# Optimization experiments

Measured on AMD Instinct MI355X. Metric: run time of the kernel, lower is better.

## Reference

```python
import jax, jax.numpy as jnp
import numpy as np

ALPHA = 0.2  # LeakyReLU negative slope


def setup_inputs() -> dict:
    key = jax.random.key(0)
    k0, k1, k2, k3 = jax.random.split(key, 4)
    N, H, W, T, V = 16, 32, 32, 16, 64
    h = jax.random.normal(k0, (N, H, W, T, V), jnp.float32)
    conv_w = jax.random.normal(k1, (3, 3, T, T), jnp.float32) * 0.05  # HWIO
    conv_b = jnp.zeros((T,), jnp.float32)
    a = jax.random.normal(k2, (2 * H * W, 1), jnp.float32) * 0.03  # ~xavier scale
    B = jax.random.uniform(k3, (V, V), jnp.float32)
    return {"h": h, "conv_w": conv_w, "conv_b": conv_b, "a": a, "B": B}


def reference(h, conv_w, conv_b, a, B):
    N, H, W, T, V = h.shape
    hv = jnp.transpose(h, (0, 4, 1, 2, 3))  # (N,V,H,W,T)

    # ConvMapping: 3x3 SAME conv over spatial dims with T as channels
    x = hv.reshape(N * V, H, W, T)
    y = jax.lax.conv_general_dilated(
        x, conv_w, (1, 1), 'SAME',
        dimension_numbers=('NHWC', 'HWIO', 'NHWC')) + conv_b
    Wh = y.reshape(N, V, H, W, T)

    # Attention logits. Original builds concat([Wh_i, Wh_j], dim=W) with trailing
    # layout (H, 2W, T) then row-major views it as (T, 2*H*W). We reproduce that
    # exact reinterpretation, but exploit additivity over i/j so the O(V^2)
    # pair tensor is never materialized.
    HW2 = 2 * H * W
    zeros = jnp.zeros_like(Wh)
    Cl = jnp.concatenate([Wh, zeros], axis=3).reshape(N, V, T, HW2)
    Cr = jnp.concatenate([zeros, Wh], axis=3).reshape(N, V, T, HW2)
    av = a[:, 0]
    Ei = jnp.einsum('bvtk,k->bvt', Cl, av)
    Ej = jnp.einsum('bvtk,k->bvt', Cr, av)
    e = jax.nn.leaky_relu(Ei[:, :, None, :] + Ej[:, None, :, :], ALPHA)  # (N,V,V,T)
    att = jax.nn.softmax(e, axis=-1)  # softmax over time dim, as in original

    # Symmetric-normalized adjacency: D^-1/2 (B + I, min-max scaled) D^-1/2
    adj = B + jnp.eye(V, dtype=B.dtype)
    adj = (adj - adj.min()) / (adj.max() - adj.min())
    d12 = 1.0 / jnp.sqrt(jnp.sum(adj, axis=1))
    adj_norm = adj * d12[:, None] * d12[None, :]

    # Aggregation: h_prime[b,p,t,i] = sum_j Wh[b,j,p,t] * att[b,i,j,t]
    # (replaces the original V^2 python loop + diag_embed matmuls)
    Whf = Wh.reshape(N, V, H * W, T)
    hp = jnp.einsum('bjpt,bijt->bpti', Whf, att)  # (N,HW,T,V)
    out = jnp.einsum('bpti,iv->bptv', hp, adj_norm)
    return jax.nn.elu(out.reshape(N, H, W, T, V))
```

## Files before the change

### kernel.cpp

```cpp
#include <hip/hip_runtime.h>
#include <hip/hip_bf16.h>
#include <math.h>

#define ALPHA_ 0.2f
#define N_ 16
#define H_ 32
#define W_ 32
#define T_ 16
#define V_ 64
#define P_ (H_*W_)

typedef __bf16 bf16x8 __attribute__((ext_vector_type(8)));
typedef float  f32x4  __attribute__((ext_vector_type(4)));

static __device__ inline bf16x8 zero8() {
    bf16x8 z;
    #pragma unroll
    for (int i = 0; i < 8; ++i) z[i] = (__bf16)0.f;
    return z;
}

static __device__ inline unsigned short bf16bits(float f) {
    __hip_bfloat16 b = __float2bfloat16(f);
    return *reinterpret_cast<unsigned short*>(&b);
}

static __device__ inline __bf16 tobf(float f) {
    unsigned short u = bf16bits(f);
    return *reinterpret_cast<__bf16*>(&u);
}

__global__ __launch_bounds__(256) void conv_k(const float* __restrict__ X,
                                              const float* __restrict__ CW,
                                              const float* __restrict__ CB,
                                              const float* __restrict__ av,
                                              __hip_bfloat16* __restrict__ Whb,
                                              float* __restrict__ Eihi,
                                              float* __restrict__ Eihj) {
    __shared__ __align__(16) __hip_bfloat16 sx[3*32*2*16*8];
    __shared__ float sEi[4][16], sEj[4][16];

    int orig = blockIdx.x;
    int bi   = (orig & 7) * 256 + (orig >> 3);
    int b    = bi >> 7;
    int rem  = bi & 127;
    int h    = rem >> 2;
    int vg   = rem & 3, vb = vg * 16;

    int tid = threadIdx.x, lane = tid & 63, wc = tid >> 6;
    int lm = lane & 15, kg = lane >> 4;

    bf16x8 Bf01[3], Bf2[3];
    #pragma unroll
    for (int dw = 0; dw < 3; ++dw) {
        #pragma unroll
        for (int i = 0; i < 8; ++i) {
            int ti = (kg & 1)*8 + i;
            int dh = kg >> 1;
            Bf01[dw][i] = tobf(CW[((dh*3+dw)*16+ti)*16 + lm]);
            Bf2 [dw][i] = (kg < 2) ? tobf(CW[((6+dw)*16+ti)*16 + lm]) : (__bf16)0.f;
        }
    }
    float cb = CB[lm];
    f32x4 acc[8];
    #pragma unroll
    for (int wi = 0; wi < 8; ++wi) acc[wi] = (f32x4){cb, cb, cb, cb};

    unsigned* sxw = (unsigned*)sx;
    int v4i = tid & 3, tiP = (tid >> 2) & 7, sub = tid >> 5;
    const float* Xbase = X + (size_t)b*(H_*W_*T_*V_) + (size_t)(2*tiP)*V_ + vb + v4i*4;
    #pragma unroll
    for (int it = 0; it < 12; ++it) {
        int rest = it*8 + sub;
        int w = rest & 31, r = rest >> 5;
        int hy = h - 1 + r;
        f32x4 xa = {0.f,0.f,0.f,0.f}, xb = {0.f,0.f,0.f,0.f};
        if ((unsigned)hy < (unsigned)H_) {
            const float* p = Xbase + ((size_t)hy*W_ + w)*(T_*V_);
            xa = *(const f32x4*)(p);
            xb = *(const f32x4*)(p + V_);
        }
        int widx = ((r*32 + w)*2 + (tiP>>2))*64 + v4i*16 + (tiP & 3);
        #pragma unroll
        for (int k2 = 0; k2 < 4; ++k2) {
            unsigned pk = (unsigned)bf16bits(xa[k2]) | ((unsigned)bf16bits(xb[k2]) << 16);
            sxw[widx + k2*4] = pk;
        }
    }
    __syncthreads();

    const char* sxb = (const char*)sx;
    int off01 = (kg>>1)*16384 + (kg&1)*256 + lm*16;
    int off2  = 2*16384       + (kg&1)*256 + lm*16;

    #pragma unroll
    for (int u = 0; u < 10; ++u) {
        int wxu = wc*8 + u - 1;
        bf16x8 f01 = zero8(), f2 = zero8();
        if ((unsigned)wxu < (unsigned)W_) {
            f01 = *(const bf16x8*)(sxb + off01 + wxu*512);
            f2  = *(const bf16x8*)(sxb + off2  + wxu*512);
        }
        #pragma unroll
        for (int dw = 0; dw < 3; ++dw) {
            int wi = u - dw;
            if (wi >= 0 && wi < 8) {
                acc[wi] = __builtin_amdgcn_mfma_f32_16x16x32_bf16(f01, Bf01[dw], acc[wi], 0, 0, 0);
                acc[wi] = __builtin_amdgcn_mfma_f32_16x16x32_bf16(f2,  Bf2 [dw], acc[wi], 0, 0, 0);
            }
        }
    }

    float si[4] = {0.f,0.f,0.f,0.f}, sj[4] = {0.f,0.f,0.f,0.f};
    {
        const float* avb = av + (h & 1)*1024 + wc*8*16 + lm;
        #pragma unroll
        for (int wi = 0; wi < 8; ++wi) {
            float ai = avb[wi*16];
            float aj = avb[wi*16 + 512];
            #pragma unroll
            for (int r = 0; r < 4; ++r) {
                si[r] += acc[wi][r] * ai;
                sj[r] += acc[wi][r] * aj;
            }
        }
        #pragma unroll
        for (int off = 1; off < 16; off <<= 1) {
            #pragma unroll
            for (int r = 0; r < 4; ++r) {
                si[r] += __shfl_xor(si[r], off);
                sj[r] += __shfl_xor(sj[r], off);
            }
        }
    }
    if (lm == 0) {
        #pragma unroll
        for (int r = 0; r < 4; ++r) {
            sEi[wc][kg*4 + r] = si[r];
            sEj[wc][kg*4 + r] = sj[r];
        }
    }

    #pragma unroll
    for (int wi = 0; wi < 8; ++wi) {
        int p = h*W_ + wc*8 + wi;
        unsigned short u0 = bf16bits(acc[wi][0]);
        unsigned short u1 = bf16bits(acc[wi][1]);
        unsigned short u2 = bf16bits(acc[wi][2]);
        unsigned short u3 = bf16bits(acc[wi][3]);
        uint2 pk;
        pk.x = (unsigned)u0 | ((unsigned)u1 << 16);
        pk.y = (unsigned)u2 | ((unsigned)u3 << 16);
        *(uint2*)(Whb + ((size_t)(b*T_ + lm)*P_ + p)*V_ + vb + kg*4) = pk;
    }

    __syncthreads();
    if (tid < 16) {
        float a = sEi[0][tid] + sEi[1][tid] + sEi[2][tid] + sEi[3][tid];
        float c = sEj[0][tid] + sEj[1][tid] + sEj[2][tid] + sEj[3][tid];
        Eihi[((size_t)b*H_ + h)*V_ + vb + tid] = a;
        Eihj[((size_t)b*H_ + h)*V_ + vb + tid] = c;
    }
}

__global__ __launch_bounds__(256) void att_m_k(const float* __restrict__ Eihi,
                                               const float* __restrict__ Eihj,
                                               const float* __restrict__ Bm,
                                               __hip_bfloat16* __restrict__ Mt) {
    int b = blockIdx.x >> 6;
    int j = blockIdx.x & 63;
    int tid = threadIdx.x;
    __shared__ float sadj[64][65];
    __shared__ float s_att[64][17];
    __shared__ float sd[64];

    if (tid < 64) {
        int i = tid;
        for (int r = 0; r < 64; ++r) sadj[r][i] = Bm[r*64 + i];
        float mn = 1e30f, mx = -1e30f;
        #pragma unroll
        for (int v = 0; v < 64; ++v) {
            float x = sadj[i][v] + (v == i ? 1.f : 0.f);
            mn = fminf(mn, x);
            mx = fmaxf(mx, x);
        }
        #pragma unroll
        for (int off = 32; off > 0; off >>= 1) {
            mn = fminf(mn, __shfl_xor(mn, off));
            mx = fmaxf(mx, __shfl_xor(mx, off));
        }
        float inv = 1.f / (mx - mn);
        float rs = 0.f;
        #pragma unroll
        for (int v = 0; v < 64; ++v) {
            float x = (sadj[i][v] + (v == i ? 1.f : 0.f) - mn) * inv;
            rs += x;
            sadj[i][v] = x;
        }
        float d = rsqrtf(rs);
        sd[i] = d;

        const float* ebi = Eihi + (size_t)b*H_*V_;
        const float* ebj = Eihj + (size_t)b*H_*V_;
        float ev[16];
        float mxe = -1e30f;
        #pragma unroll
        for (int t = 0; t < 16; ++t) {
            float x = ebi[(2*t)*V_ + i] + ebi[(2*t+1)*V_ + i]
                    + ebj[(2*t)*V_ + j] + ebj[(2*t+1)*V_ + j];
            x = (x >= 0.f) ? x : ALPHA_ * x;
            ev[t] = x;
            mxe = fmaxf(mxe, x);
        }
        float s = 0.f;
        #pragma unroll
        for (int t = 0; t < 16; ++t) {
            ev[t] = __expf(ev[t] - mxe);
            s += ev[t];
        }
        float invs = d / s;
        #pragma unroll
        for (int t = 0; t < 16; ++t) s_att[i][t] = ev[t] * invs;
    }
    __syncthreads();

    int v = tid & 63, tq = tid >> 6;
    float acc[4] = {0.f, 0.f, 0.f, 0.f};
    for (int i = 0; i < 64; ++i) {
        float an = sadj[i][v];
        #pragma unroll
        for (int u = 0; u < 4; ++u) acc[u] += s_att[i][tq*4 + u] * an;
    }
    float dv = sd[v];
    #pragma unroll
    for (int u = 0; u < 4; ++u) {
        int t = tq*4 + u;
        Mt[(((size_t)b*T_ + t)*V_ + v)*V_ + j] = __float2bfloat16(acc[u] * dv);
    }
}

__global__ __launch_bounds__(256) void out_k(const __hip_bfloat16* __restrict__ Whb,
                                             const __hip_bfloat16* __restrict__ Mt,
                                             float* __restrict__ out) {
    int bi = blockIdx.x;
    int pc = bi & 7;
    int t  = (bi >> 3) & 15;
    int b  = bi >> 7;

    int tid  = threadIdx.x;
    int lane = tid & 63;
    int wid  = tid >> 6;
    int lm   = lane & 15;
    int lk   = lane >> 4;

    const __hip_bfloat16* Ab = Whb + ((size_t)(b*T_ + t)*P_ + pc*128) * V_;
    const __hip_bfloat16* Bb = Mt  + (size_t)(b*T_ + t) * (V_*V_);

    f32x4 acc[2][4];
    #pragma unroll
    for (int pt = 0; pt < 2; ++pt)
        #pragma unroll
        for (int vt = 0; vt < 4; ++vt) acc[pt][vt] = (f32x4){0.f,0.f,0.f,0.f};

    #pragma unroll
    for (int kf = 0; kf < 2; ++kf) {
        int ko = kf*32 + lk*8;
        bf16x8 a0 = *(const bf16x8*)(Ab + ((size_t)((wid*2+0)*16 + lm))*V_ + ko);
        bf16x8 a1 = *(const bf16x8*)(Ab + ((size_t)((wid*2+1)*16 + lm))*V_ + ko);
        #pragma unroll
        for (int vt = 0; vt < 4; ++vt) {
            bf16x8 bf = *(const bf16x8*)(Bb + ((size_t)(vt*16 + lm))*V_ + ko);
            acc[0][vt] = __builtin_amdgcn_mfma_f32_16x16x32_bf16(a0, bf, acc[0][vt], 0, 0, 0);
            acc[1][vt] = __builtin_amdgcn_mfma_f32_16x16x32_bf16(a1, bf, acc[1][vt], 0, 0, 0);
        }
    }

    #pragma unroll
    for (int pt = 0; pt < 2; ++pt) {
        #pragma unroll
        for (int vt = 0; vt < 4; ++vt) {
            #pragma unroll
            for (int r = 0; r < 4; ++r) {
                int p  = pc*128 + (wid*2 + pt)*16 + lk*4 + r;
                int vv = vt*16 + lm;
                float x = acc[pt][vt][r];
                x = (x > 0.f) ? x : (__expf(x) - 1.f);
                out[((size_t)(b*P_ + p)*T_ + t)*V_ + vv] = x;
            }
        }
    }
}

extern "C" void kernel_launch(void* const* d_in, const int* in_sizes, int n_in,
                              void* d_out, int out_size, void* d_ws, size_t ws_size,
                              hipStream_t stream) {
    const float* X  = (const float*)d_in[0];
    const float* CW = (const float*)d_in[1];
    const float* CB = (const float*)d_in[2];
    const float* av = (const float*)d_in[3];
    const float* Bm = (const float*)d_in[4];
    float* outp = (float*)d_out;

    __hip_bfloat16* Whb = (__hip_bfloat16*)d_ws;
    __hip_bfloat16* Mt  = Whb + (size_t)N_*T_*P_*V_;
    float* Eihi = (float*)(Mt + (size_t)N_*T_*V_*V_);
    float* Eihj = Eihi + (size_t)N_*H_*V_;

    conv_k <<<2048,    256, 0, stream>>>(X, CW, CB, av, Whb, Eihi, Eihj);
    att_m_k<<<N_*V_,   256, 0, stream>>>(Eihi, Eihj, Bm, Mt);
    out_k  <<<N_*T_*8, 256, 0, stream>>>(Whb, Mt, outp);
}
```

Baseline: 82.51 us.

## Batch conv input loads into registers and XOR-swizzle LDS tile layout

The conv kernel now issues all twelve global loads into register arrays before converting and storing to LDS, so more memory requests are in flight at once. The LDS layout is XOR-swizzled by w parity and t-half so stores and MFMA fragment reads avoid bank conflicts, with the read offsets adjusted to match. Launch bounds request two blocks per CU. The extra registers held by the batched loads may cost occupancy or cause spills.

```diff
diff --git a/kernel.cpp b/kernel.cpp
--- a/kernel.cpp
+++ b/kernel.cpp
@@ -30,13 +30,13 @@
     return *reinterpret_cast<__bf16*>(&u);
 }
 
-__global__ __launch_bounds__(256) void conv_k(const float* __restrict__ X,
-                                              const float* __restrict__ CW,
-                                              const float* __restrict__ CB,
-                                              const float* __restrict__ av,
-                                              __hip_bfloat16* __restrict__ Whb,
-                                              float* __restrict__ Eihi,
-                                              float* __restrict__ Eihj) {
+__global__ __launch_bounds__(256, 2) void conv_k(const float* __restrict__ X,
+                                                 const float* __restrict__ CW,
+                                                 const float* __restrict__ CB,
+                                                 const float* __restrict__ av,
+                                                 __hip_bfloat16* __restrict__ Whb,
+                                                 float* __restrict__ Eihi,
+                                                 float* __restrict__ Eihj) {
     __shared__ __align__(16) __hip_bfloat16 sx[3*32*2*16*8];
     __shared__ float sEi[4][16], sEj[4][16];
 
@@ -68,38 +68,54 @@
 
     unsigned* sxw = (unsigned*)sx;
     int v4i = tid & 3, tiP = (tid >> 2) & 7, sub = tid >> 5;
+    int th  = tiP >> 2, tpl = tiP & 3;
     const float* Xbase = X + (size_t)b*(H_*W_*T_*V_) + (size_t)(2*tiP)*V_ + vb + v4i*4;
+
+    f32x4 xa[12], xb[12];
     #pragma unroll
     for (int it = 0; it < 12; ++it) {
         int rest = it*8 + sub;
         int w = rest & 31, r = rest >> 5;
         int hy = h - 1 + r;
-        f32x4 xa = {0.f,0.f,0.f,0.f}, xb = {0.f,0.f,0.f,0.f};
+        xa[it] = (f32x4){0.f,0.f,0.f,0.f};
+        xb[it] = (f32x4){0.f,0.f,0.f,0.f};
         if ((unsigned)hy < (unsigned)H_) {
             const float* p = Xbase + ((size_t)hy*W_ + w)*(T_*V_);
-            xa = *(const f32x4*)(p);
-            xb = *(const f32x4*)(p + V_);
-        }
-        int widx = ((r*32 + w)*2 + (tiP>>2))*64 + v4i*16 + (tiP & 3);
+            xa[it] = *(const f32x4*)(p);
+            xb[it] = *(const f32x4*)(p + V_);
+        }
+    }
+    #pragma unroll
+    for (int it = 0; it < 12; ++it) {
+        int rest = it*8 + sub;
+        int w = rest & 31, r = rest >> 5;
+        int seg = (r*32 + w)*2 + th;
+        int swz = th ^ ((w & 1) << 1);
         #pragma unroll
         for (int k2 = 0; k2 < 4; ++k2) {
-            unsigned pk = (unsigned)bf16bits(xa[k2]) | ((unsigned)bf16bits(xb[k2]) << 16);
-            sxw[widx + k2*4] = pk;
+            int gs = (v4i*4 + k2) ^ swz;
+            unsigned pk = (unsigned)bf16bits(xa[it][k2])
+                        | ((unsigned)bf16bits(xb[it][k2]) << 16);
+            sxw[seg*64 + gs*4 + tpl] = pk;
         }
     }
     __syncthreads();
 
     const char* sxb = (const char*)sx;
-    int off01 = (kg>>1)*16384 + (kg&1)*256 + lm*16;
-    int off2  = 2*16384       + (kg&1)*256 + lm*16;
+    int lmx  = (lm ^ (kg & 1)) * 16;
+    int o01A = (kg>>1)*16384 + (kg&1)*256 + lmx;
+    int o01B = o01A ^ 32;
+    int o2A  = 2*16384 + (kg&1)*256 + lmx;
+    int o2B  = o2A ^ 32;
 
     #pragma unroll
     for (int u = 0; u < 10; ++u) {
         int wxu = wc*8 + u - 1;
+        const int oddw = (u + 1) & 1;
         bf16x8 f01 = zero8(), f2 = zero8();
         if ((unsigned)wxu < (unsigned)W_) {
-            f01 = *(const bf16x8*)(sxb + off01 + wxu*512);
-            f2  = *(const bf16x8*)(sxb + off2  + wxu*512);
+            f01 = *(const bf16x8*)(sxb + (oddw ? o01B : o01A) + wxu*512);
+            f2  = *(const bf16x8*)(sxb + (oddw ? o2B  : o2A ) + wxu*512);
         }
         #pragma unroll
         for (int dw = 0; dw < 3; ++dw) {
```

New measurement: 78.59 us. 4.8% less time.

## Split conv over two channel halves with register prefetch and swizzled LDS

Applied to the files above, without the earlier changes.

Restructures the conv kernel to process the 16 input channels in two halves of 8. The second half's global loads are issued into registers while the first half's MFMAs run. This halves the shared-memory tile, packs the three kernel rows into the K dimension of each MFMA, and adds an XOR swizzle on LDS writes and reads to cut bank conflicts. With the smaller LDS tile it also requests three blocks per CU through launch bounds, at the cost of extra barriers and more live registers for the prefetched data.

```diff
diff --git a/kernel.cpp b/kernel.cpp
--- a/kernel.cpp
+++ b/kernel.cpp
@@ -30,14 +30,14 @@
     return *reinterpret_cast<__bf16*>(&u);
 }
 
-__global__ __launch_bounds__(256) void conv_k(const float* __restrict__ X,
-                                              const float* __restrict__ CW,
-                                              const float* __restrict__ CB,
-                                              const float* __restrict__ av,
-                                              __hip_bfloat16* __restrict__ Whb,
-                                              float* __restrict__ Eihi,
-                                              float* __restrict__ Eihj) {
-    __shared__ __align__(16) __hip_bfloat16 sx[3*32*2*16*8];
+__global__ __launch_bounds__(256, 3) void conv_k(const float* __restrict__ X,
+                                                 const float* __restrict__ CW,
+                                                 const float* __restrict__ CB,
+                                                 const float* __restrict__ av,
+                                                 __hip_bfloat16* __restrict__ Whb,
+                                                 float* __restrict__ Eihi,
+                                                 float* __restrict__ Eihj) {
+    __shared__ __align__(16) __hip_bfloat16 sx[3*32*128];
     __shared__ float sEi[4][16], sEj[4][16];
 
     int orig = blockIdx.x;
@@ -50,64 +50,120 @@
     int tid = threadIdx.x, lane = tid & 63, wc = tid >> 6;
     int lm = lane & 15, kg = lane >> 4;
 
-    bf16x8 Bf01[3], Bf2[3];
-    #pragma unroll
-    for (int dw = 0; dw < 3; ++dw) {
-        #pragma unroll
-        for (int i = 0; i < 8; ++i) {
-            int ti = (kg & 1)*8 + i;
-            int dh = kg >> 1;
-            Bf01[dw][i] = tobf(CW[((dh*3+dw)*16+ti)*16 + lm]);
-            Bf2 [dw][i] = (kg < 2) ? tobf(CW[((6+dw)*16+ti)*16 + lm]) : (__bf16)0.f;
-        }
-    }
+    int v4i = tid & 3;
+    int tp  = (tid >> 2) & 3;
+    int sub = tid >> 4;
+    const float* Xb = X + (size_t)b*(H_*W_*T_*V_) + vb + v4i*4;
+    unsigned* sxw = (unsigned*)sx;
+    int cth = sub & 3;
+
+    f32x4 xa0[6], xb0[6];
+    #pragma unroll
+    for (int it = 0; it < 6; ++it) {
+        int r = it >> 1, w = (it & 1)*16 + sub;
+        int hy = h - 1 + r;
+        xa0[it] = (f32x4){0.f,0.f,0.f,0.f};
+        xb0[it] = (f32x4){0.f,0.f,0.f,0.f};
+        if ((unsigned)hy < (unsigned)H_) {
+            const float* p = Xb + ((size_t)hy*W_ + w)*(T_*V_) + (2*tp)*V_;
+            xa0[it] = *(const f32x4*)(p);
+            xb0[it] = *(const f32x4*)(p + V_);
+        }
+    }
+
+    bf16x8 Bf[2][3];
+    #pragma unroll
+    for (int p = 0; p < 2; ++p)
+        #pragma unroll
+        for (int dw = 0; dw < 3; ++dw)
+            #pragma unroll
+            for (int i = 0; i < 8; ++i)
+                Bf[p][dw][i] = (kg < 3)
+                    ? tobf(CW[((kg*3 + dw)*16 + p*8 + i)*16 + lm])
+                    : (__bf16)0.f;
+
     float cb = CB[lm];
     f32x4 acc[8];
     #pragma unroll
     for (int wi = 0; wi < 8; ++wi) acc[wi] = (f32x4){cb, cb, cb, cb};
 
-    unsigned* sxw = (unsigned*)sx;
-    int v4i = tid & 3, tiP = (tid >> 2) & 7, sub = tid >> 5;
-    const float* Xbase = X + (size_t)b*(H_*W_*T_*V_) + (size_t)(2*tiP)*V_ + vb + v4i*4;
-    #pragma unroll
-    for (int it = 0; it < 12; ++it) {
-        int rest = it*8 + sub;
-        int w = rest & 31, r = rest >> 5;
+    #pragma unroll
+    for (int it = 0; it < 6; ++it) {
+        int r = it >> 1, w = (it & 1)*16 + sub;
+        int seg = r*32 + w;
+        #pragma unroll
+        for (int k2 = 0; k2 < 4; ++k2) {
+            int g = (v4i*4 + k2) ^ cth;
+            sxw[seg*64 + g*4 + tp] =
+                (unsigned)bf16bits(xa0[it][k2]) | ((unsigned)bf16bits(xb0[it][k2]) << 16);
+        }
+    }
+
+    f32x4 xa1[6], xb1[6];
+    #pragma unroll
+    for (int it = 0; it < 6; ++it) {
+        int r = it >> 1, w = (it & 1)*16 + sub;
         int hy = h - 1 + r;
-        f32x4 xa = {0.f,0.f,0.f,0.f}, xb = {0.f,0.f,0.f,0.f};
+        xa1[it] = (f32x4){0.f,0.f,0.f,0.f};
+        xb1[it] = (f32x4){0.f,0.f,0.f,0.f};
         if ((unsigned)hy < (unsigned)H_) {
-            const float* p = Xbase + ((size_t)hy*W_ + w)*(T_*V_);
-            xa = *(const f32x4*)(p);
-            xb = *(const f32x4*)(p + V_);
-        }
-        int widx = ((r*32 + w)*2 + (tiP>>2))*64 + v4i*16 + (tiP & 3);
-        #pragma unroll
-        for (int k2 = 0; k2 < 4; ++k2) {
-            unsigned pk = (unsigned)bf16bits(xa[k2]) | ((unsigned)bf16bits(xb[k2]) << 16);
-            sxw[widx + k2*4] = pk;
-        }
-    }
+            const float* p = Xb + ((size_t)hy*W_ + w)*(T_*V_) + (8 + 2*tp)*V_;
+            xa1[it] = *(const f32x4*)(p);
+            xb1[it] = *(const f32x4*)(p + V_);
+        }
+    }
+
     __syncthreads();
 
     const char* sxb = (const char*)sx;
-    int off01 = (kg>>1)*16384 + (kg&1)*256 + lm*16;
-    int off2  = 2*16384       + (kg&1)*256 + lm*16;
+    int r3 = (kg < 3) ? kg : 0;
+    int Abase = r3*8192 + lm*16;
 
     #pragma unroll
     for (int u = 0; u < 10; ++u) {
         int wxu = wc*8 + u - 1;
-        bf16x8 f01 = zero8(), f2 = zero8();
+        const int cu = (u + 3) & 3;
+        bf16x8 fA = zero8();
         if ((unsigned)wxu < (unsigned)W_) {
-            f01 = *(const bf16x8*)(sxb + off01 + wxu*512);
-            f2  = *(const bf16x8*)(sxb + off2  + wxu*512);
+            fA = *(const bf16x8*)(sxb + (Abase ^ (cu << 4)) + wxu*256);
         }
         #pragma unroll
         for (int dw = 0; dw < 3; ++dw) {
             int wi = u - dw;
-            if (wi >= 0 && wi < 8) {
-                acc[wi] = __builtin_amdgcn_mfma_f32_16x16x32_bf16(f01, Bf01[dw], acc[wi], 0, 0, 0);
-                acc[wi] = __builtin_amdgcn_mfma_f32_16x16x32_bf16(f2,  Bf2 [dw], acc[wi], 0, 0, 0);
-            }
+            if (wi >= 0 && wi < 8)
+                acc[wi] = __builtin_amdgcn_mfma_f32_16x16x32_bf16(fA, Bf[0][dw], acc[wi], 0, 0, 0);
+        }
+    }
+
+    __syncthreads();
+
+    #pragma unroll
+    for (int it = 0; it < 6; ++it) {
+        int r = it >> 1, w = (it & 1)*16 + sub;
+        int seg = r*32 + w;
+        #pragma unroll
+        for (int k2 = 0; k2 < 4; ++k2) {
+            int g = (v4i*4 + k2) ^ cth;
+            sxw[seg*64 + g*4 + tp] =
+                (unsigned)bf16bits(xa1[it][k2]) | ((unsigned)bf16bits(xb1[it][k2]) << 16);
+        }
+    }
+
+    __syncthreads();
+
+    #pragma unroll
+    for (int u = 0; u < 10; ++u) {
+        int wxu = wc*8 + u - 1;
+        const int cu = (u + 3) & 3;
+        bf16x8 fA = zero8();
+        if ((unsigned)wxu < (unsigned)W_) {
+            fA = *(const bf16x8*)(sxb + (Abase ^ (cu << 4)) + wxu*256);
+        }
+        #pragma unroll
+        for (int dw = 0; dw < 3; ++dw) {
+            int wi = u - dw;
+            if (wi >= 0 && wi < 8)
+                acc[wi] = __builtin_amdgcn_mfma_f32_16x16x32_bf16(fA, Bf[1][dw], acc[wi], 0, 0, 0);
         }
     }
 
```

New measurement: 92.57 us. 1.12x slower.

## Pre-transpose input to padded bf16 layout in separate kernel before conv

Applied to the files above, without the earlier changes.

Adds a kernel that converts the fp32 input to bf16, transposes it so T is innermost per (h,w,v), and pads H with zero rows. It writes into the output buffer as scratch. The conv kernel then loads MFMA fragments directly from global memory instead of staging a 3-row halo through shared memory. This removes the threefold redundant fp32 reads and the LDS staging, at the cost of an extra launch and an extra bf16 round trip through global memory.

```diff
diff --git a/kernel.cpp b/kernel.cpp
--- a/kernel.cpp
+++ b/kernel.cpp
@@ -30,14 +30,85 @@
     return *reinterpret_cast<__bf16*>(&u);
 }
 
-__global__ __launch_bounds__(256) void conv_k(const float* __restrict__ X,
+__global__ __launch_bounds__(256) void tr2_k(const float* __restrict__ X,
+                                             __hip_bfloat16* __restrict__ Xt) {
+    int bid = blockIdx.x;
+    int b   = bid / 136;
+    int r   = bid % 136;
+    int hp  = r >> 2;
+    int wq  = r & 3;
+    int tid = threadIdx.x;
+
+    __hip_bfloat16* dst = Xt + (((size_t)(b*34 + hp)*W_ + wq*8) * V_) * T_;
+
+    if (hp == 0 || hp == 33) {
+        uint4 z = {0u,0u,0u,0u};
+        uint4* d = (uint4*)dst;
+        #pragma unroll
+        for (int k = 0; k < 4; ++k) d[tid + 256*k] = z;
+        return;
+    }
+    int h = hp - 1;
+
+    __shared__ __align__(16) unsigned sx[4096];
+
+    int vq  = tid & 15;
+    int tp4 = (tid >> 4) & 3;
+    int w4  = tid >> 6;
+    const float* Xb = X + (((size_t)(b*H_ + h)*W_ + wq*8) * T_) * V_ + vq*4;
+
+    f32x4 xr[2][2][2];
+    #pragma unroll
+    for (int iw = 0; iw < 2; ++iw) {
+        int wl = iw*4 + w4;
+        #pragma unroll
+        for (int th = 0; th < 2; ++th) {
+            #pragma unroll
+            for (int tk = 0; tk < 2; ++tk) {
+                int ti = (th*4 + tp4)*2 + tk;
+                xr[iw][th][tk] = *(const f32x4*)(Xb + ((size_t)wl*T_ + ti)*V_);
+            }
+        }
+    }
+    #pragma unroll
+    for (int iw = 0; iw < 2; ++iw) {
+        int wl = iw*4 + w4;
+        #pragma unroll
+        for (int th = 0; th < 2; ++th) {
+            int tp = th*4 + tp4;
+            uint4 pk;
+            unsigned* pw = (unsigned*)&pk;
+            #pragma unroll
+            for (int k2 = 0; k2 < 4; ++k2)
+                pw[k2] = (unsigned)bf16bits(xr[iw][th][0][k2])
+                       | ((unsigned)bf16bits(xr[iw][th][1][k2]) << 16);
+            *(uint4*)&sx[(wl*8 + tp)*64 + (vq ^ tp4)*4] = pk;
+        }
+    }
+    __syncthreads();
+
+    #pragma unroll
+    for (int k = 0; k < 4; ++k) {
+        int c   = tid + 256*k;
+        int wl  = c >> 7;
+        int vv  = (c >> 1) & 63;
+        int thf = c & 1;
+        uint4 o;
+        unsigned* ow = (unsigned*)&o;
+        #pragma unroll
+        for (int q = 0; q < 4; ++q)
+            ow[q] = sx[(wl*8 + thf*4 + q)*64 + ((vv >> 2) ^ q)*4 + (vv & 3)];
+        *(uint4*)(dst + ((size_t)wl*V_ + vv)*T_ + thf*8) = o;
+    }
+}
+
+__global__ __launch_bounds__(256) void conv_k(const __hip_bfloat16* __restrict__ Xt,
                                               const float* __restrict__ CW,
                                               const float* __restrict__ CB,
                                               const float* __restrict__ av,
                                               __hip_bfloat16* __restrict__ Whb,
                                               float* __restrict__ Eihi,
                                               float* __restrict__ Eihj) {
-    __shared__ __align__(16) __hip_bfloat16 sx[3*32*2*16*8];
     __shared__ float sEi[4][16], sEj[4][16];
 
     int orig = blockIdx.x;
@@ -66,40 +137,18 @@
     #pragma unroll
     for (int wi = 0; wi < 8; ++wi) acc[wi] = (f32x4){cb, cb, cb, cb};
 
-    unsigned* sxw = (unsigned*)sx;
-    int v4i = tid & 3, tiP = (tid >> 2) & 7, sub = tid >> 5;
-    const float* Xbase = X + (size_t)b*(H_*W_*T_*V_) + (size_t)(2*tiP)*V_ + vb + v4i*4;
-    #pragma unroll
-    for (int it = 0; it < 12; ++it) {
-        int rest = it*8 + sub;
-        int w = rest & 31, r = rest >> 5;
-        int hy = h - 1 + r;
-        f32x4 xa = {0.f,0.f,0.f,0.f}, xb = {0.f,0.f,0.f,0.f};
-        if ((unsigned)hy < (unsigned)H_) {
-            const float* p = Xbase + ((size_t)hy*W_ + w)*(T_*V_);
-            xa = *(const f32x4*)(p);
-            xb = *(const f32x4*)(p + V_);
-        }
-        int widx = ((r*32 + w)*2 + (tiP>>2))*64 + v4i*16 + (tiP & 3);
-        #pragma unroll
-        for (int k2 = 0; k2 < 4; ++k2) {
-            unsigned pk = (unsigned)bf16bits(xa[k2]) | ((unsigned)bf16bits(xb[k2]) << 16);
-            sxw[widx + k2*4] = pk;
-        }
-    }
-    __syncthreads();
-
-    const char* sxb = (const char*)sx;
-    int off01 = (kg>>1)*16384 + (kg&1)*256 + lm*16;
-    int off2  = 2*16384       + (kg&1)*256 + lm*16;
+    const __hip_bfloat16* base01 =
+        Xt + ((size_t)((b*34 + h + (kg>>1))*W_)*V_ + vb + lm)*T_ + (kg&1)*8;
+    const __hip_bfloat16* base2  =
+        Xt + ((size_t)((b*34 + h + 2)*W_)*V_ + vb + lm)*T_ + (kg&1)*8;
 
     #pragma unroll
     for (int u = 0; u < 10; ++u) {
         int wxu = wc*8 + u - 1;
         bf16x8 f01 = zero8(), f2 = zero8();
         if ((unsigned)wxu < (unsigned)W_) {
-            f01 = *(const bf16x8*)(sxb + off01 + wxu*512);
-            f2  = *(const bf16x8*)(sxb + off2  + wxu*512);
+            f01 = *(const bf16x8*)(base01 + (size_t)wxu*(V_*T_));
+            f2  = *(const bf16x8*)(base2  + (size_t)wxu*(V_*T_));
         }
         #pragma unroll
         for (int dw = 0; dw < 3; ++dw) {
@@ -306,7 +355,10 @@
     float* Eihi = (float*)(Mt + (size_t)N_*T_*V_*V_);
     float* Eihj = Eihi + (size_t)N_*H_*V_;
 
-    conv_k <<<2048,    256, 0, stream>>>(X, CW, CB, av, Whb, Eihi, Eihj);
+    __hip_bfloat16* Xt = (__hip_bfloat16*)d_out;
+
+    tr2_k  <<<N_*34*4, 256, 0, stream>>>(X, Xt);
+    conv_k <<<2048,    256, 0, stream>>>(Xt, CW, CB, av, Whb, Eihi, Eihj);
     att_m_k<<<N_*V_,   256, 0, stream>>>(Eihi, Eihj, Bm, Mt);
     out_k  <<<N_*T_*8, 256, 0, stream>>>(Whb, Mt, outp);
 }
```

Result: slower. 85.85 us (+4.0%).
